# Kernel tuning notes

Hardware: AMD Instinct MI355X
Metric: run time of the kernel (lower is better)

The kernel has to match this reference:

```python
import jax, jax.numpy as jnp
import numpy as np

D_MODEL = 256
D_STATE = 64
HEADDIM = 64
EXPAND = 2
D_INNER = EXPAND * D_MODEL        # 512
D_SSM = D_INNER                   # 512
NGROUPS = 1
NHEADS = D_SSM // HEADDIM         # 8
CONV_DIM = D_SSM + 2 * NGROUPS * D_STATE   # 640
D_IN_PROJ = 2 * D_INNER + 2 * NGROUPS * D_STATE + NHEADS  # 1160
BATCH, Himg, Wimg = 8, 64, 64
EPS = 1e-5


def causal_dw_conv1d(x, w, b):
    """Depthwise causal conv1d + SiLU. x:(B,C,L), w:(C,K), b:(C,)"""
    K = w.shape[1]
    L = x.shape[-1]
    xp = jnp.pad(x, ((0, 0), (0, 0), (K - 1, 0)))
    y = b[None, :, None]
    for k in range(K):
        y = y + w[:, k][None, :, None] * xp[:, :, k:k + L]
    return jax.nn.silu(y)


def setup_inputs() -> dict:
    key = jax.random.key(0)
    ks = jax.random.split(key, 12)
    u = jax.random.normal(ks[0], (BATCH, D_MODEL, Himg, Wimg), jnp.float32)
    in_proj_w = jax.random.normal(ks[1], (D_IN_PROJ, D_MODEL), jnp.float32) * 0.02
    conv_dt_w = jax.random.normal(ks[2], (NHEADS, 4), jnp.float32) * 0.1
    # dt_bias via inverse-softplus of dt ~ logU(1e-3, 0.1) as in the module init
    dt0 = jnp.exp(jax.random.uniform(ks[3], (NHEADS,)) * (np.log(0.1) - np.log(0.001)) + np.log(0.001))
    dt_bias = dt0 + jnp.log(-jnp.expm1(-dt0))
    conv_xBC_w = jax.random.normal(ks[4], (CONV_DIM, 3), jnp.float32) * 0.1
    conv_xBC_b = jax.random.normal(ks[5], (CONV_DIM,), jnp.float32) * 0.02
    conv_z_w = jax.random.normal(ks[6], (D_SSM, 3), jnp.float32) * 0.1
    conv_z_b = jax.random.normal(ks[7], (D_SSM,), jnp.float32) * 0.02
    A_log = jnp.log(jax.random.uniform(ks[8], (NHEADS,), minval=1.0, maxval=16.0))
    D_param = jnp.ones((NHEADS,), jnp.float32)
    norm_w = jnp.ones((D_SSM,), jnp.float32)
    out_proj_w = jax.random.normal(ks[9], (D_MODEL, D_SSM, 3, 3), jnp.float32) * 0.02
    return {"u": u, "in_proj_w": in_proj_w, "conv_dt_w": conv_dt_w, "dt_bias": dt_bias,
            "conv_xBC_w": conv_xBC_w, "conv_xBC_b": conv_xBC_b,
            "conv_z_w": conv_z_w, "conv_z_b": conv_z_b,
            "A_log": A_log, "D_param": D_param, "norm_w": norm_w, "out_proj_w": out_proj_w}


def reference(u, in_proj_w, conv_dt_w, dt_bias, conv_xBC_w, conv_xBC_b,
              conv_z_w, conv_z_b, A_log, D_param, norm_w, out_proj_w):
    B, C, H, W = u.shape
    L = H * W
    # 1x1 conv in_proj -> (B, D_IN_PROJ, L)
    zxbcdt = jnp.einsum('oc,bchw->bohw', in_proj_w, u).reshape(B, D_IN_PROJ, L)
    z = zxbcdt[:, :D_SSM]                                  # (B, D_SSM, L)
    xBC = zxbcdt[:, D_SSM:D_SSM + CONV_DIM]                # (B, CONV_DIM, L)
    dt = zxbcdt[:, D_SSM + CONV_DIM:]                      # (B, NHEADS, L)

    A = -jnp.exp(A_log)                                    # (NHEADS,)
    dt = causal_dw_conv1d(dt, conv_dt_w, dt_bias)          # (B, H, L), silu'd
    xBC = causal_dw_conv1d(xBC, conv_xBC_w, conv_xBC_b)    # (B, CONV_DIM, L)

    x = xBC[:, :D_SSM]                                     # (B, D_SSM, L)
    Bm = jnp.transpose(xBC[:, D_SSM:D_SSM + D_STATE], (0, 2, 1))   # (B, L, N)
    Cm = jnp.transpose(xBC[:, D_SSM + D_STATE:], (0, 2, 1))        # (B, L, N)

    # x: (B, h*c, L) -> V: (B, h, L, c)
    V = jnp.transpose(x.reshape(B, NHEADS, HEADDIM, L), (0, 1, 3, 2))
    # dA = dt * A per head: (B, h, L, 1)
    dA = dt[:, :, :, None] * A[None, :, None, None]
    V_scaled = V * dA
    # non-causal linear attention duality (ngroups==1)
    KV = jnp.einsum('bln,bhld->bhnd', Bm, V_scaled)        # (B, h, N, d)
    y = jnp.einsum('bln,bhnd->bhld', Cm, KV) + V * D_param[None, :, None, None]
    y = jnp.transpose(y, (0, 2, 1, 3)).reshape(B, L, D_SSM)

    # gate branch
    zc = causal_dw_conv1d(z, conv_z_w, conv_z_b)           # (B, D_SSM, L)
    zc = jnp.transpose(zc, (0, 2, 1))                      # (B, L, D_SSM)
    # RMSNormGated, norm_before_gate=False: gate first then normalize
    yg = y * jax.nn.silu(zc)
    yn = yg * jax.lax.rsqrt(jnp.mean(yg * yg, axis=-1, keepdims=True) + EPS) * norm_w

    y_img = jnp.transpose(yn, (0, 2, 1)).reshape(B, D_SSM, H, W)
    out = jax.lax.conv_general_dilated(y_img, out_proj_w, (1, 1), 'SAME',
                                       dimension_numbers=('NCHW', 'OIHW', 'NCHW'))
    return out
```

## Files before the change

kernel.cpp:

```cpp
#include <hip/hip_runtime.h>
#include <math.h>


constexpr int BATCH  = 8;
constexpr int CIN    = 256;
constexpr int HH     = 64, WW = 64;
constexpr int L      = HH * WW;
constexpr int DPROJ  = 1160;
constexpr int DSSM   = 512;
constexpr int DSTATE = 64;
constexpr int NH     = 8;
constexpr int HD     = 64;
constexpr int CONVD  = 640;
constexpr int COUT   = 256;
constexpr float EPS  = 1e-5f;

typedef __attribute__((ext_vector_type(8))) short short8;
typedef __attribute__((ext_vector_type(4))) float f32x4;

static __device__ __forceinline__ float silu_f(float x) {
    return x / (1.f + __expf(-x));
}
static __device__ __forceinline__ float bf2f(unsigned short u) {
    return __uint_as_float(((unsigned)u) << 16);
}
static __device__ __forceinline__ unsigned short f2bf(float f) {
    unsigned x = __float_as_uint(f);
    unsigned r = (x + 0x7FFFu + ((x >> 16) & 1u)) >> 16;
    return (unsigned short)r;
}

static __device__ __forceinline__ void gl2lds16(const unsigned short* g, short* l) {
    __builtin_amdgcn_global_load_lds(
        (const __attribute__((address_space(1))) unsigned int*)g,
        (__attribute__((address_space(3))) unsigned int*)l, 16, 0, 0);
}

__global__ __launch_bounds__(256) void k_wb2(const float* __restrict__ W,
                                             unsigned short* __restrict__ Wt2) {
    int idx8 = blockIdx.x * 256 + threadIdx.x;
    int tile = idx8 >> 9;
    int within = (idx8 & 511) * 8;
    int row = within >> 5;
    int slp = (within >> 3) & 3;
    int oblk = tile >> 3, ks = tile & 7;
    int o = oblk * 128 + row;
    int c = ks * 32 + (slp ^ (row & 3)) * 8;
    unsigned short s[8] = {0, 0, 0, 0, 0, 0, 0, 0};
    if (o < DPROJ) {
        float4 v0 = *(const float4*)(W + (size_t)o * CIN + c);
        float4 v1 = *(const float4*)(W + (size_t)o * CIN + c + 4);
        s[0] = f2bf(v0.x); s[1] = f2bf(v0.y); s[2] = f2bf(v0.z); s[3] = f2bf(v0.w);
        s[4] = f2bf(v1.x); s[5] = f2bf(v1.y); s[6] = f2bf(v1.z); s[7] = f2bf(v1.w);
    }
    *(uint4*)(Wt2 + (size_t)tile * 4096 + within) = *(uint4*)s;
}

__global__ __launch_bounds__(256) void k_uT(const float* __restrict__ u,
                                            unsigned short* __restrict__ uTt) {
    __shared__ float Ts[32][33];
    int l0 = blockIdx.x * 32;
    int c0 = blockIdx.y * 32;
    int b  = blockIdx.z;
    int tid = threadIdx.x;
    {
        int r = tid >> 3, c4 = tid & 7;
        float4 v = *(const float4*)(u + ((size_t)b * CIN + c0 + r) * L + l0 + c4 * 4);
        Ts[r][c4 * 4 + 0] = v.x;
        Ts[r][c4 * 4 + 1] = v.y;
        Ts[r][c4 * 4 + 2] = v.z;
        Ts[r][c4 * 4 + 3] = v.w;
    }
    __syncthreads();
    {
        int lr = tid >> 3, cg = tid & 7;
        unsigned short s[4];
#pragma unroll
        for (int j = 0; j < 4; ++j) s[j] = f2bf(Ts[cg * 4 + j][lr]);
        int lg = l0 + lr;
        int tile = ((b * 32 + (lg >> 7)) << 3) + (c0 >> 5);
        int row = lg & 127;
        int slot = (cg >> 1) ^ (row & 3);
        size_t off = (size_t)tile * 4096 + row * 32 + slot * 8 + (cg & 1) * 4;
        *(uint2*)(uTt + off) = *(uint2*)s;
    }
}

__global__ __launch_bounds__(256) void k_wprep(const float* __restrict__ Wt,
                                               unsigned short* __restrict__ Wb2) {
    int i = blockIdx.x * 256 + threadIdx.x;
    int co = i >> 9, ci = i & 511;
    const float* src = Wt + (size_t)i * 9;
#pragma unroll
    for (int tap = 0; tap < 9; ++tap) {
        Wb2[(((size_t)tap * 64 + (ci >> 3)) * 256 + co) * 8 + (ci & 7)] = f2bf(src[tap]);
    }
}

__global__ __launch_bounds__(256) void k_inprojm(const unsigned short* __restrict__ Wt2,
                                                 const unsigned short* __restrict__ uTt,
                                                 unsigned short* __restrict__ zx) {
    __shared__ short Ab[2][4096];
    __shared__ short Bbuf[2][4096];
    int lblk = blockIdx.x, oblk = blockIdx.y, b = blockIdx.z;
    int tid = threadIdx.x, lane = tid & 63, w = tid >> 6;
    int laneN = lane & 15, laneK = lane >> 4;

    const unsigned short* At = uTt + (size_t)(b * 32 + lblk) * 8 * 4096;
    const unsigned short* Bt = Wt2 + (size_t)oblk * 8 * 4096;

    f32x4 acc[4][4];
#pragma unroll
    for (int mt = 0; mt < 4; ++mt)
#pragma unroll
        for (int nt = 0; nt < 4; ++nt) acc[mt][nt] = (f32x4){0.f, 0.f, 0.f, 0.f};

    gl2lds16(At + tid * 8,        &Ab[0][tid * 8]);
    gl2lds16(At + 2048 + tid * 8, &Ab[0][2048 + tid * 8]);
    gl2lds16(Bt + tid * 8,        &Bbuf[0][tid * 8]);
    gl2lds16(Bt + 2048 + tid * 8, &Bbuf[0][2048 + tid * 8]);
    __syncthreads();

    int arow = (w & 1) * 64;
    int brow = (w >> 1) * 64;
    int asl = (laneK ^ (laneN & 3)) * 8;

    int cur = 0;
    for (int ks = 0; ks < 8; ++ks) {
        if (ks < 7) {
            const unsigned short* an = At + (size_t)(ks + 1) * 4096;
            const unsigned short* bn = Bt + (size_t)(ks + 1) * 4096;
            int c2 = cur ^ 1;
            gl2lds16(an + tid * 8,        &Ab[c2][tid * 8]);
            gl2lds16(an + 2048 + tid * 8, &Ab[c2][2048 + tid * 8]);
            gl2lds16(bn + tid * 8,        &Bbuf[c2][tid * 8]);
            gl2lds16(bn + 2048 + tid * 8, &Bbuf[c2][2048 + tid * 8]);
        }
        short8 av[4], bv[4];
#pragma unroll
        for (int mt = 0; mt < 4; ++mt)
            av[mt] = *(const short8*)&Ab[cur][(arow + mt * 16 + laneN) * 32 + asl];
#pragma unroll
        for (int nt = 0; nt < 4; ++nt)
            bv[nt] = *(const short8*)&Bbuf[cur][(brow + nt * 16 + laneN) * 32 + asl];
#pragma unroll
        for (int mt = 0; mt < 4; ++mt)
#pragma unroll
            for (int nt = 0; nt < 4; ++nt)
                acc[mt][nt] = __builtin_amdgcn_mfma_f32_16x16x32_bf16(av[mt], bv[nt], acc[mt][nt], 0, 0, 0);
        __syncthreads();
        cur ^= 1;
    }

    unsigned short* zb = zx + (size_t)b * DPROJ * L;
    int lbase = lblk * 128 + arow;
#pragma unroll
    for (int nt = 0; nt < 4; ++nt) {
        int o = oblk * 128 + brow + nt * 16 + laneN;
        if (o < DPROJ) {
#pragma unroll
            for (int mt = 0; mt < 4; ++mt) {
                unsigned short s[4] = {f2bf(acc[mt][nt].x), f2bf(acc[mt][nt].y),
                                       f2bf(acc[mt][nt].z), f2bf(acc[mt][nt].w)};
                *(uint2*)(zb + (size_t)o * L + lbase + mt * 16 + laneK * 4) = *(uint2*)s;
            }
        }
    }
}

__global__ __launch_bounds__(256) void k_dtdA(const unsigned short* __restrict__ zx,
                                              const float* __restrict__ cw,
                                              const float* __restrict__ cb,
                                              const float* __restrict__ Alog,
                                              float* __restrict__ dA) {
    int idx = blockIdx.x * 256 + threadIdx.x;
    int l = idx & (L - 1);
    int h = (idx >> 12) & (NH - 1);
    int b = idx >> 15;
    const unsigned short* row = zx + ((size_t)b * DPROJ + DSSM + CONVD + h) * L;
    float y = cb[h];
#pragma unroll
    for (int k = 0; k < 4; ++k) {
        int ls = l + k - 3;
        if (ls >= 0) y += cw[h * 4 + k] * bf2f(row[ls]);
    }
    dA[idx] = silu_f(y) * (-__expf(Alog[h]));
}

__global__ __launch_bounds__(256) void k_xbc(const unsigned short* __restrict__ zx,
                                             const float* __restrict__ cw,
                                             const float* __restrict__ cb,
                                             unsigned short* __restrict__ xbc) {
    int idx = blockIdx.x * 256 + threadIdx.x;
    int lg = idx & (L / 8 - 1);
    int c  = (idx >> 9) % CONVD;
    int b  = idx / (CONVD * (L / 8));
    int l0 = lg * 8;
    const unsigned short* row = zx + ((size_t)b * DPROJ + DSSM + c) * L;
    float x[10];
    uint4 raw = *(const uint4*)(row + l0);
    const unsigned short* s = (const unsigned short*)&raw;
#pragma unroll
    for (int t = 0; t < 8; ++t) x[2 + t] = bf2f(s[t]);
    if (l0 > 0) { x[0] = bf2f(row[l0 - 2]); x[1] = bf2f(row[l0 - 1]); }
    else        { x[0] = 0.f; x[1] = 0.f; }
    float w0 = cw[c * 3 + 0], w1 = cw[c * 3 + 1], w2 = cw[c * 3 + 2], bb = cb[c];
    uint4 o;
    unsigned short* os = (unsigned short*)&o;
#pragma unroll
    for (int t = 0; t < 8; ++t) {
        float y = bb + w0 * x[t] + w1 * x[t + 1] + w2 * x[t + 2];
        os[t] = f2bf(silu_f(y));
    }
    *(uint4*)(xbc + ((size_t)b * CONVD + c) * L + l0) = o;
}

__global__ __launch_bounds__(256) void k_ct(const unsigned short* __restrict__ xbc,
                                            unsigned short* __restrict__ CT) {
    __shared__ short Ts[32][33];
    int l0 = blockIdx.x * 32;
    int n0 = blockIdx.y * 32;
    int b  = blockIdx.z;
    int tid = threadIdx.x;
    {
        int r = tid >> 3, q = tid & 7;
        uint2 v = *(const uint2*)(xbc + ((size_t)b * CONVD + DSSM + DSTATE + n0 + r) * L + l0 + q * 4);
        const unsigned short* s = (const unsigned short*)&v;
#pragma unroll
        for (int t = 0; t < 4; ++t) Ts[r][q * 4 + t] = (short)s[t];
    }
    __syncthreads();
    {
        int lr = tid >> 3, qn = tid & 7;
        unsigned short s[4];
#pragma unroll
        for (int t = 0; t < 4; ++t) s[t] = (unsigned short)Ts[qn * 4 + t][lr];
        *(uint2*)(CT + ((size_t)b * L + l0 + lr) * DSTATE + n0 + qn * 4) = *(uint2*)s;
    }
}

__global__ __launch_bounds__(256) void k_kvm(const unsigned short* __restrict__ xbc,
                                             const float* __restrict__ dA,
                                             float* __restrict__ pKV) {
    __shared__ float red[4][4096];
    int kc = blockIdx.x, h = blockIdx.y, b = blockIdx.z;
    int tid = threadIdx.x, lane = tid & 63, w = tid >> 6;
    int laneN = lane & 15, laneK = lane >> 4;

    const unsigned short* Bb = xbc + ((size_t)b * CONVD + DSSM) * L;
    const unsigned short* Vb = xbc + ((size_t)b * CONVD + h * HD) * L;
    const float* dAp = dA + ((size_t)b * NH + h) * L;

    f32x4 acc[4][4];
#pragma unroll
    for (int mt = 0; mt < 4; ++mt)
#pragma unroll
        for (int nt = 0; nt < 4; ++nt) acc[mt][nt] = (f32x4){0.f, 0.f, 0.f, 0.f};

    int kbase = kc * 512 + w * 128;
#pragma unroll
    for (int ks = 0; ks < 4; ++ks) {
        int kl = kbase + ks * 32 + laneK * 8;
        float4 da0 = *(const float4*)(dAp + kl);
        float4 da1 = *(const float4*)(dAp + kl + 4);
        float dav[8] = {da0.x, da0.y, da0.z, da0.w, da1.x, da1.y, da1.z, da1.w};
        short8 afr[4];
#pragma unroll
        for (int mt = 0; mt < 4; ++mt) {
            uint4 raw = *(const uint4*)(Bb + (size_t)(mt * 16 + laneN) * L + kl);
            const unsigned short* s = (const unsigned short*)&raw;
            short8 af;
#pragma unroll
            for (int j = 0; j < 8; ++j) af[j] = (short)f2bf(bf2f(s[j]) * dav[j]);
            afr[mt] = af;
        }
#pragma unroll
        for (int nt = 0; nt < 4; ++nt) {
            short8 bfr = *(const short8*)(Vb + (size_t)(nt * 16 + laneN) * L + kl);
#pragma unroll
            for (int mt = 0; mt < 4; ++mt)
                acc[mt][nt] = __builtin_amdgcn_mfma_f32_16x16x32_bf16(afr[mt], bfr, acc[mt][nt], 0, 0, 0);
        }
    }

#pragma unroll
    for (int mt = 0; mt < 4; ++mt)
#pragma unroll
        for (int nt = 0; nt < 4; ++nt)
#pragma unroll
            for (int j = 0; j < 4; ++j)
                red[w][(mt * 16 + laneK * 4 + j) * 64 + nt * 16 + laneN] = acc[mt][nt][j];
    __syncthreads();

    float* dst = pKV + (((size_t)(b * NH + h) * 8 + kc) * 4096);
#pragma unroll
    for (int q = 0; q < 4; ++q) {
        int off = q * 1024 + tid * 4;
        float4 s0 = *(const float4*)&red[0][off];
        float4 s1 = *(const float4*)&red[1][off];
        float4 s2 = *(const float4*)&red[2][off];
        float4 s3 = *(const float4*)&red[3][off];
        float4 r;
        r.x = s0.x + s1.x + s2.x + s3.x;
        r.y = s0.y + s1.y + s2.y + s3.y;
        r.z = s0.z + s1.z + s2.z + s3.z;
        r.w = s0.w + s1.w + s2.w + s3.w;
        *(float4*)(dst + off) = r;
    }
}

__global__ __launch_bounds__(256) void k_kvred(const float* __restrict__ pKV,
                                               float* __restrict__ KV) {
    int flat4 = blockIdx.x * 256 + threadIdx.x;
    int bh = flat4 >> 10;
    int nd = (flat4 & 1023) * 4;
    float4 r = make_float4(0.f, 0.f, 0.f, 0.f);
#pragma unroll
    for (int kc = 0; kc < 8; ++kc) {
        float4 v = *(const float4*)(pKV + ((size_t)bh * 8 + kc) * 4096 + nd);
        r.x += v.x; r.y += v.y; r.z += v.z; r.w += v.w;
    }
    *(float4*)(KV + (size_t)bh * 4096 + nd) = r;
}

__global__ __launch_bounds__(256) void k_kvT(const float* __restrict__ KV,
                                             unsigned short* __restrict__ KVt) {
    __shared__ float Ts[64][65];
    int bh = blockIdx.x;
    int tid = threadIdx.x;
    const float* src = KV + (size_t)bh * 4096;
#pragma unroll
    for (int j = 0; j < 16; ++j) {
        int idx = j * 256 + tid;
        Ts[idx >> 6][idx & 63] = src[idx];
    }
    __syncthreads();
    unsigned short* dst = KVt + (size_t)bh * 4096;
#pragma unroll
    for (int j = 0; j < 4; ++j) {
        int idx = j * 256 + tid;
        int d = idx >> 4, q = idx & 15;
        unsigned short s[4];
#pragma unroll
        for (int t = 0; t < 4; ++t) s[t] = f2bf(Ts[q * 4 + t][d]);
        *(uint2*)(dst + d * 64 + q * 4) = *(uint2*)s;
    }
}

__global__ __launch_bounds__(256) void k_y5am(const unsigned short* __restrict__ CT,
                                              const unsigned short* __restrict__ KVt,
                                              const unsigned short* __restrict__ xbc,
                                              const unsigned short* __restrict__ zx,
                                              const float* __restrict__ zw,
                                              const float* __restrict__ zb,
                                              const float* __restrict__ Dp,
                                              unsigned short* __restrict__ ygout) {
    int l0 = blockIdx.x * 128;
    int h  = blockIdx.y;
    int b  = blockIdx.z;
    int tid = threadIdx.x, lane = tid & 63, w = tid >> 6;
    int laneN = lane & 15, laneK = lane >> 4;
    int lw = l0 + w * 32;

    const unsigned short* ctb = CT + (size_t)b * L * DSTATE;
    const unsigned short* kvb = KVt + ((size_t)b * NH + h) * HD * DSTATE;

    f32x4 acc[2][4];
#pragma unroll
    for (int mt = 0; mt < 2; ++mt)
#pragma unroll
        for (int nt = 0; nt < 4; ++nt) acc[mt][nt] = (f32x4){0.f, 0.f, 0.f, 0.f};

#pragma unroll
    for (int ks = 0; ks < 2; ++ks) {
        int ko = ks * 32 + laneK * 8;
        short8 av[2], bv[4];
#pragma unroll
        for (int mt = 0; mt < 2; ++mt)
            av[mt] = *(const short8*)(ctb + (size_t)(lw + mt * 16 + laneN) * DSTATE + ko);
#pragma unroll
        for (int nt = 0; nt < 4; ++nt)
            bv[nt] = *(const short8*)(kvb + (size_t)(nt * 16 + laneN) * DSTATE + ko);
#pragma unroll
        for (int mt = 0; mt < 2; ++mt)
#pragma unroll
            for (int nt = 0; nt < 4; ++nt)
                acc[mt][nt] = __builtin_amdgcn_mfma_f32_16x16x32_bf16(av[mt], bv[nt], acc[mt][nt], 0, 0, 0);
    }

    const unsigned short* xb = xbc + (size_t)b * CONVD * L;
    float Dh = Dp[h];
#pragma unroll
    for (int nt = 0; nt < 4; ++nt) {
        int d = nt * 16 + laneN;
        int c = h * HD + d;
        float w0 = zw[c * 3 + 0], w1 = zw[c * 3 + 1], w2 = zw[c * 3 + 2];
        float bz = zb[c];
        const unsigned short* vrow = xb + (size_t)c * L;
        const unsigned short* zrow = zx + ((size_t)b * DPROJ + c) * L;
#pragma unroll
        for (int mt = 0; mt < 2; ++mt) {
            int lpos = lw + mt * 16 + laneK * 4;
            float v[4];
            {
                uint2 raw = *(const uint2*)(vrow + lpos);
                const unsigned short* s = (const unsigned short*)&raw;
#pragma unroll
                for (int t = 0; t < 4; ++t) v[t] = bf2f(s[t]);
            }
            float zv[8];
            if (lpos >= 4) {
                uint2 z0 = *(const uint2*)(zrow + lpos - 4);
                const unsigned short* s = (const unsigned short*)&z0;
#pragma unroll
                for (int t = 0; t < 4; ++t) zv[t] = bf2f(s[t]);
            } else {
                zv[0] = zv[1] = zv[2] = zv[3] = 0.f;
            }
            {
                uint2 z1 = *(const uint2*)(zrow + lpos);
                const unsigned short* s = (const unsigned short*)&z1;
#pragma unroll
                for (int t = 0; t < 4; ++t) zv[4 + t] = bf2f(s[t]);
            }
            unsigned short sp[4];
#pragma unroll
            for (int j = 0; j < 4; ++j) {
                float y = acc[mt][nt][j] + v[j] * Dh;
                float zy = bz + w0 * zv[j + 2] + w1 * zv[j + 3] + w2 * zv[j + 4];
                sp[j] = f2bf(y * silu_f(silu_f(zy)));
            }
            *(uint2*)(ygout + (size_t)b * DPROJ * L + (size_t)c * L + lpos) = *(uint2*)sp;
        }
    }
}

constexpr int R_LT = 32;

__global__ __launch_bounds__(256) void k_y5bT(const unsigned short* __restrict__ yg,
                                              const float* __restrict__ nw,
                                              unsigned short* __restrict__ ynT) {
    __shared__ float ygs[DSSM][R_LT + 1];
    __shared__ float red[8][R_LT];
    __shared__ float rs[R_LT];
    int l0 = blockIdx.x * R_LT;
    int b  = blockIdx.y;
    int tid = threadIdx.x;
    int ll = tid & 31, grp = tid >> 5;
    const unsigned short* ygb = yg + (size_t)b * DPROJ * L;
#pragma unroll
    for (int j = 0; j < 64; ++j) {
        int i = j * 256 + tid;
        int c = i >> 5, lc = i & 31;
        ygs[c][lc] = bf2f(ygb[(size_t)c * L + l0 + lc]);
    }
    __syncthreads();
    float ss = 0.f;
#pragma unroll
    for (int ci = 0; ci < 64; ++ci) {
        float t = ygs[grp * 64 + ci][ll];
        ss += t * t;
    }
    red[grp][ll] = ss;
    __syncthreads();
    if (tid < R_LT) {
        float s = 0.f;
#pragma unroll
        for (int g = 0; g < 8; ++g) s += red[g][tid];
        rs[tid] = rsqrtf(s * (1.f / DSSM) + EPS);
    }
    __syncthreads();
    int lc = tid & 31, cg = tid >> 5;
    float r = rs[lc];
    unsigned short* dst = ynT + ((size_t)b * L + l0 + lc) * DSSM + cg * 64;
#pragma unroll
    for (int j = 0; j < 8; ++j) {
        uint4 pk;
        unsigned short* sp = (unsigned short*)&pk;
#pragma unroll
        for (int t = 0; t < 8; ++t) {
            int c = cg * 64 + j * 8 + t;
            sp[t] = f2bf(ygs[c][lc] * r * nw[c]);
        }
        *(uint4*)(dst + j * 8) = pk;
    }
}

__global__ __launch_bounds__(256, 4) void k_conv3m(const unsigned short* __restrict__ ynT,
                                                   const unsigned short* __restrict__ Wb2,
                                                   float* __restrict__ out) {
    __shared__ short Alds[4 * 66 * 72];
    int h0  = blockIdx.x * 2;
    int co0 = blockIdx.y * 64;
    int b   = blockIdx.z;
    int tid  = threadIdx.x;
    int lane = tid & 63;
    int wid  = tid >> 6;
    int wm = wid >> 1, wn = wid & 1;
    int laneN = lane & 15, laneK = lane >> 4;

    f32x4 acc[4][2];
#pragma unroll
    for (int mt = 0; mt < 4; ++mt)
#pragma unroll
        for (int nt = 0; nt < 2; ++nt) acc[mt][nt] = (f32x4){0.f, 0.f, 0.f, 0.f};

    const unsigned short* ynb = ynT + (size_t)b * L * DSSM;

    const int a_wi1 = tid >> 2, a_sl = tid & 3;

    if (tid < 64) {
        int rw = tid >> 3, q = tid & 7;
        int r = rw >> 1, wi = (rw & 1) ? 65 : 0;
        *(uint4*)&Alds[(r * 66 + wi) * 72 + q * 8] = make_uint4(0u, 0u, 0u, 0u);
    }

    uint4 pA[8];
#pragma unroll
    for (int j = 0; j < 4; ++j) {
        int hrow = h0 - 1 + j;
        bool ok = (hrow >= 0 && hrow < HH);
        const unsigned short* src = ynb + (size_t)(hrow * WW + a_wi1) * DSSM;
#pragma unroll
        for (int s2 = 0; s2 < 2; ++s2) {
            pA[j * 2 + s2] = make_uint4(0u, 0u, 0u, 0u);
            if (ok) pA[j * 2 + s2] = *(const uint4*)(src + (a_sl + s2 * 4) * 8);
        }
    }

    const unsigned short* wbp =
        Wb2 + ((size_t)laneK * 256 + co0 + wn * 32 + laneN) * 8;

    for (int ci0 = 0; ci0 < DSSM; ci0 += 64) {
        __syncthreads();
#pragma unroll
        for (int j = 0; j < 4; ++j)
#pragma unroll
            for (int s2 = 0; s2 < 2; ++s2)
                *(uint4*)&Alds[(j * 66 + a_wi1 + 1) * 72 + (a_sl + s2 * 4) * 8] = pA[j * 2 + s2];
        __syncthreads();

        if (ci0 + 64 < DSSM) {
            int cin = ci0 + 64;
#pragma unroll
            for (int j = 0; j < 4; ++j) {
                int hrow = h0 - 1 + j;
                bool ok = (hrow >= 0 && hrow < HH);
                const unsigned short* src = ynb + (size_t)(hrow * WW + a_wi1) * DSSM + cin;
#pragma unroll
                for (int s2 = 0; s2 < 2; ++s2) {
                    pA[j * 2 + s2] = make_uint4(0u, 0u, 0u, 0u);
                    if (ok) pA[j * 2 + s2] = *(const uint4*)(src + (a_sl + s2 * 4) * 8);
                }
            }
        }

        const unsigned short* wbc = wbp + (size_t)(ci0 >> 3) * 2048;
        short8 bC[4];
#pragma unroll
        for (int ks = 0; ks < 2; ++ks)
#pragma unroll
            for (int nt = 0; nt < 2; ++nt)
                bC[ks * 2 + nt] = *(const short8*)(wbc + (size_t)ks * 8192 + nt * 128);
#pragma unroll
        for (int tap = 0; tap < 9; ++tap) {
            short8 bN[4];
#pragma unroll
            for (int q = 0; q < 4; ++q) bN[q] = bC[q];
            if (tap < 8) {
#pragma unroll
                for (int ks = 0; ks < 2; ++ks)
#pragma unroll
                    for (int nt = 0; nt < 2; ++nt)
                        bN[ks * 2 + nt] = *(const short8*)(wbc + (size_t)(tap + 1) * 131072 +
                                                          (size_t)ks * 8192 + nt * 128);
            }
            const int kh = tap / 3, kw = tap % 3;
#pragma unroll
            for (int ks = 0; ks < 2; ++ks) {
#pragma unroll
                for (int mt = 0; mt < 4; ++mt) {
                    short8 af = *(const short8*)&Alds[((wm + kh) * 66 + laneN + mt * 16 + kw) * 72 +
                                                      (laneK + ks * 4) * 8];
                    acc[mt][0] = __builtin_amdgcn_mfma_f32_16x16x32_bf16(af, bC[ks * 2 + 0], acc[mt][0], 0, 0, 0);
                    acc[mt][1] = __builtin_amdgcn_mfma_f32_16x16x32_bf16(af, bC[ks * 2 + 1], acc[mt][1], 0, 0, 0);
                }
            }
#pragma unroll
            for (int q = 0; q < 4; ++q) bC[q] = bN[q];
        }
    }

    float* ob = out + (size_t)b * COUT * L + (size_t)(h0 + wm) * WW;
#pragma unroll
    for (int mt = 0; mt < 4; ++mt) {
#pragma unroll
        for (int nt = 0; nt < 2; ++nt) {
            int co = co0 + wn * 32 + nt * 16 + laneN;
            float4 v = make_float4(acc[mt][nt].x, acc[mt][nt].y, acc[mt][nt].z, acc[mt][nt].w);
            *(float4*)(ob + (size_t)co * L + mt * 16 + laneK * 4) = v;
        }
    }
}

extern "C" void kernel_launch(void* const* d_in, const int* in_sizes, int n_in,
                              void* d_out, int out_size, void* d_ws, size_t ws_size,
                              hipStream_t stream) {
    const float* u          = (const float*)d_in[0];
    const float* in_proj_w  = (const float*)d_in[1];
    const float* conv_dt_w  = (const float*)d_in[2];
    const float* dt_bias    = (const float*)d_in[3];
    const float* conv_xBC_w = (const float*)d_in[4];
    const float* conv_xBC_b = (const float*)d_in[5];
    const float* conv_z_w   = (const float*)d_in[6];
    const float* conv_z_b   = (const float*)d_in[7];
    const float* A_log      = (const float*)d_in[8];
    const float* D_param    = (const float*)d_in[9];
    const float* norm_w     = (const float*)d_in[10];
    const float* out_w      = (const float*)d_in[11];
    float* out = (float*)d_out;

    const size_t n_zx  = (size_t)BATCH * DPROJ * L;
    const size_t n_xbc = (size_t)BATCH * CONVD * L;
    const size_t n_yn  = (size_t)BATCH * DSSM * L;
    const size_t n_dA  = (size_t)BATCH * NH * L;
    const size_t n_KV  = (size_t)BATCH * NH * DSTATE * HD;
    const size_t n_pKV = (size_t)BATCH * NH * 8 * DSTATE * HD;
    const size_t n_Wb2 = (size_t)9 * 64 * 256 * 8;
    const size_t n_ct  = (size_t)BATCH * L * DSTATE;
    const size_t n_kvt = (size_t)BATCH * NH * HD * DSTATE;
    const size_t need  = 2 * (n_zx + n_xbc + n_yn + n_Wb2 + n_ct + n_kvt)
                       + 4 * (n_dA + n_KV + n_pKV);
    if (ws_size < need) return;

    unsigned short* zx  = (unsigned short*)d_ws;
    unsigned short* xbc = zx + n_zx;
    unsigned short* ynT = xbc + n_xbc;
    float*          dAb = (float*)(ynT + n_yn);
    float*          KV  = dAb + n_dA;
    float*          pKV = KV + n_KV;
    unsigned short* Wb2 = (unsigned short*)(pKV + n_pKV);
    unsigned short* CT  = Wb2 + n_Wb2;
    unsigned short* KVt = CT + n_ct;
    unsigned short* uTt  = ynT;
    unsigned short* Wt2  = (unsigned short*)pKV;
    unsigned short* ygbuf = zx + (size_t)DSSM * L;

    k_wb2<<<160, 256, 0, stream>>>(in_proj_w, Wt2);

    dim3 gt(L / 32, CIN / 32, BATCH);
    k_uT<<<gt, 256, 0, stream>>>(u, uTt);

    k_wprep<<<(COUT * DSSM) / 256, 256, 0, stream>>>(out_w, Wb2);

    dim3 g1(L / 128, 10, BATCH);
    k_inprojm<<<g1, 256, 0, stream>>>(Wt2, uTt, zx);

    k_dtdA<<<BATCH * NH * L / 256, 256, 0, stream>>>(zx, conv_dt_w, dt_bias, A_log, dAb);

    k_xbc<<<BATCH * CONVD * (L / 8) / 256, 256, 0, stream>>>(zx, conv_xBC_w, conv_xBC_b, xbc);

    dim3 gct(L / 32, DSTATE / 32, BATCH);
    k_ct<<<gct, 256, 0, stream>>>(xbc, CT);

    dim3 g4(8, NH, BATCH);
    k_kvm<<<g4, 256, 0, stream>>>(xbc, dAb, pKV);
    k_kvred<<<256, 256, 0, stream>>>(pKV, KV);
    k_kvT<<<BATCH * NH, 256, 0, stream>>>(KV, KVt);

    dim3 g5(L / 128, NH, BATCH);
    k_y5am<<<g5, 256, 0, stream>>>(CT, KVt, xbc, zx, conv_z_w, conv_z_b, D_param, ygbuf);

    dim3 g5b(L / R_LT, BATCH);
    k_y5bT<<<g5b, 256, 0, stream>>>(ygbuf, norm_w, ynT);

    dim3 g6(HH / 2, COUT / 64, BATCH);
    k_conv3m<<<g6, 256, 0, stream>>>(ynT, Wb2, out);
}
```

Before: 248.0 us.

## Fuse KV reduction with transpose, and fuse y-gating with RMSNorm into one kernel

The partial-KV reduction is merged into the transpose/bf16 conversion kernel, and the y computation (C·KV plus D skip and z gate) is fused with the RMSNorm into a single kernel. Each block now covers all 8 heads for 32 positions, so the row sum of squares is reduced in registers, by shuffles and through a small shared array, instead of passing through an intermediate yg buffer. This removes two launches and the round trip of the gated activations through global memory. The cost is that ynT is written with scattered 2-byte stores strided by DSSM, and the KV reduction now runs on only 64 blocks.

```diff
diff --git a/kernel.cpp b/kernel.cpp
--- a/kernel.cpp
+++ b/kernel.cpp
@@ -309,30 +309,19 @@
     }
 }
 
-__global__ __launch_bounds__(256) void k_kvred(const float* __restrict__ pKV,
-                                               float* __restrict__ KV) {
-    int flat4 = blockIdx.x * 256 + threadIdx.x;
-    int bh = flat4 >> 10;
-    int nd = (flat4 & 1023) * 4;
-    float4 r = make_float4(0.f, 0.f, 0.f, 0.f);
-#pragma unroll
-    for (int kc = 0; kc < 8; ++kc) {
-        float4 v = *(const float4*)(pKV + ((size_t)bh * 8 + kc) * 4096 + nd);
-        r.x += v.x; r.y += v.y; r.z += v.z; r.w += v.w;
-    }
-    *(float4*)(KV + (size_t)bh * 4096 + nd) = r;
-}
-
-__global__ __launch_bounds__(256) void k_kvT(const float* __restrict__ KV,
-                                             unsigned short* __restrict__ KVt) {
+__global__ __launch_bounds__(256) void k_kvrt(const float* __restrict__ pKV,
+                                              unsigned short* __restrict__ KVt) {
     __shared__ float Ts[64][65];
     int bh = blockIdx.x;
     int tid = threadIdx.x;
-    const float* src = KV + (size_t)bh * 4096;
+    const float* src = pKV + (size_t)bh * 8 * 4096;
 #pragma unroll
     for (int j = 0; j < 16; ++j) {
         int idx = j * 256 + tid;
-        Ts[idx >> 6][idx & 63] = src[idx];
+        float s = 0.f;
+#pragma unroll
+        for (int kc = 0; kc < 8; ++kc) s += src[(size_t)kc * 4096 + idx];
+        Ts[idx >> 6][idx & 63] = s;
     }
     __syncthreads();
     unsigned short* dst = KVt + (size_t)bh * 4096;
@@ -347,60 +336,65 @@
     }
 }
 
-__global__ __launch_bounds__(256) void k_y5am(const unsigned short* __restrict__ CT,
-                                              const unsigned short* __restrict__ KVt,
-                                              const unsigned short* __restrict__ xbc,
-                                              const unsigned short* __restrict__ zx,
-                                              const float* __restrict__ zw,
-                                              const float* __restrict__ zb,
-                                              const float* __restrict__ Dp,
-                                              unsigned short* __restrict__ ygout) {
-    int l0 = blockIdx.x * 128;
-    int h  = blockIdx.y;
-    int b  = blockIdx.z;
+__global__ __launch_bounds__(256) void k_y5n(const unsigned short* __restrict__ CT,
+                                             const unsigned short* __restrict__ KVt,
+                                             const unsigned short* __restrict__ xbc,
+                                             const unsigned short* __restrict__ zx,
+                                             const float* __restrict__ zw,
+                                             const float* __restrict__ zb,
+                                             const float* __restrict__ Dp,
+                                             const float* __restrict__ nw,
+                                             unsigned short* __restrict__ ynT) {
+    __shared__ float red[32][4];
+    int l0 = blockIdx.x * 32;
+    int b  = blockIdx.y;
     int tid = threadIdx.x, lane = tid & 63, w = tid >> 6;
     int laneN = lane & 15, laneK = lane >> 4;
-    int lw = l0 + w * 32;
 
     const unsigned short* ctb = CT + (size_t)b * L * DSTATE;
-    const unsigned short* kvb = KVt + ((size_t)b * NH + h) * HD * DSTATE;
-
-    f32x4 acc[2][4];
+    const unsigned short* xb  = xbc + (size_t)b * CONVD * L;
+
+    f32x4 acc[2][8];
 #pragma unroll
     for (int mt = 0; mt < 2; ++mt)
 #pragma unroll
-        for (int nt = 0; nt < 4; ++nt) acc[mt][nt] = (f32x4){0.f, 0.f, 0.f, 0.f};
+        for (int nt = 0; nt < 8; ++nt) acc[mt][nt] = (f32x4){0.f, 0.f, 0.f, 0.f};
 
 #pragma unroll
     for (int ks = 0; ks < 2; ++ks) {
         int ko = ks * 32 + laneK * 8;
-        short8 av[2], bv[4];
+        short8 av[2];
 #pragma unroll
         for (int mt = 0; mt < 2; ++mt)
-            av[mt] = *(const short8*)(ctb + (size_t)(lw + mt * 16 + laneN) * DSTATE + ko);
-#pragma unroll
-        for (int nt = 0; nt < 4; ++nt)
-            bv[nt] = *(const short8*)(kvb + (size_t)(nt * 16 + laneN) * DSTATE + ko);
-#pragma unroll
-        for (int mt = 0; mt < 2; ++mt)
-#pragma unroll
-            for (int nt = 0; nt < 4; ++nt)
-                acc[mt][nt] = __builtin_amdgcn_mfma_f32_16x16x32_bf16(av[mt], bv[nt], acc[mt][nt], 0, 0, 0);
-    }
-
-    const unsigned short* xb = xbc + (size_t)b * CONVD * L;
-    float Dh = Dp[h];
-#pragma unroll
-    for (int nt = 0; nt < 4; ++nt) {
-        int d = nt * 16 + laneN;
-        int c = h * HD + d;
+            av[mt] = *(const short8*)(ctb + (size_t)(l0 + mt * 16 + laneN) * DSTATE + ko);
+#pragma unroll
+        for (int nt = 0; nt < 8; ++nt) {
+            int head = w * 2 + (nt >> 2);
+            const unsigned short* kvb = KVt + (size_t)(b * NH + head) * (HD * DSTATE);
+            short8 bv = *(const short8*)(kvb + (size_t)((nt & 3) * 16 + laneN) * DSTATE + ko);
+            acc[0][nt] = __builtin_amdgcn_mfma_f32_16x16x32_bf16(av[0], bv, acc[0][nt], 0, 0, 0);
+            acc[1][nt] = __builtin_amdgcn_mfma_f32_16x16x32_bf16(av[1], bv, acc[1][nt], 0, 0, 0);
+        }
+    }
+
+    float ps[2][4];
+#pragma unroll
+    for (int mt = 0; mt < 2; ++mt)
+#pragma unroll
+        for (int j = 0; j < 4; ++j) ps[mt][j] = 0.f;
+
+#pragma unroll
+    for (int nt = 0; nt < 8; ++nt) {
+        int head = w * 2 + (nt >> 2);
+        int c = head * 64 + (nt & 3) * 16 + laneN;
+        float Dh = Dp[head];
         float w0 = zw[c * 3 + 0], w1 = zw[c * 3 + 1], w2 = zw[c * 3 + 2];
         float bz = zb[c];
         const unsigned short* vrow = xb + (size_t)c * L;
         const unsigned short* zrow = zx + ((size_t)b * DPROJ + c) * L;
 #pragma unroll
         for (int mt = 0; mt < 2; ++mt) {
-            int lpos = lw + mt * 16 + laneK * 4;
+            int lpos = l0 + mt * 16 + laneK * 4;
             float v[4];
             {
                 uint2 raw = *(const uint2*)(vrow + lpos);
@@ -423,66 +417,56 @@
 #pragma unroll
                 for (int t = 0; t < 4; ++t) zv[4 + t] = bf2f(s[t]);
             }
-            unsigned short sp[4];
 #pragma unroll
             for (int j = 0; j < 4; ++j) {
                 float y = acc[mt][nt][j] + v[j] * Dh;
                 float zy = bz + w0 * zv[j + 2] + w1 * zv[j + 3] + w2 * zv[j + 4];
-                sp[j] = f2bf(y * silu_f(silu_f(zy)));
-            }
-            *(uint2*)(ygout + (size_t)b * DPROJ * L + (size_t)c * L + lpos) = *(uint2*)sp;
-        }
-    }
-}
-
-constexpr int R_LT = 32;
-
-__global__ __launch_bounds__(256) void k_y5bT(const unsigned short* __restrict__ yg,
-                                              const float* __restrict__ nw,
-                                              unsigned short* __restrict__ ynT) {
-    __shared__ float ygs[DSSM][R_LT + 1];
-    __shared__ float red[8][R_LT];
-    __shared__ float rs[R_LT];
-    int l0 = blockIdx.x * R_LT;
-    int b  = blockIdx.y;
-    int tid = threadIdx.x;
-    int ll = tid & 31, grp = tid >> 5;
-    const unsigned short* ygb = yg + (size_t)b * DPROJ * L;
-#pragma unroll
-    for (int j = 0; j < 64; ++j) {
-        int i = j * 256 + tid;
-        int c = i >> 5, lc = i & 31;
-        ygs[c][lc] = bf2f(ygb[(size_t)c * L + l0 + lc]);
+                float yg = y * silu_f(silu_f(zy));
+                ps[mt][j] += yg * yg;
+                acc[mt][nt][j] = yg;
+            }
+        }
+    }
+
+#pragma unroll
+    for (int m = 1; m <= 8; m <<= 1) {
+#pragma unroll
+        for (int mt = 0; mt < 2; ++mt)
+#pragma unroll
+            for (int j = 0; j < 4; ++j)
+                ps[mt][j] += __shfl_xor(ps[mt][j], m, 64);
+    }
+    if (laneN == 0) {
+#pragma unroll
+        for (int mt = 0; mt < 2; ++mt)
+#pragma unroll
+            for (int j = 0; j < 4; ++j)
+                red[mt * 16 + laneK * 4 + j][w] = ps[mt][j];
     }
     __syncthreads();
-    float ss = 0.f;
-#pragma unroll
-    for (int ci = 0; ci < 64; ++ci) {
-        float t = ygs[grp * 64 + ci][ll];
-        ss += t * t;
-    }
-    red[grp][ll] = ss;
-    __syncthreads();
-    if (tid < R_LT) {
-        float s = 0.f;
-#pragma unroll
-        for (int g = 0; g < 8; ++g) s += red[g][tid];
-        rs[tid] = rsqrtf(s * (1.f / DSSM) + EPS);
-    }
-    __syncthreads();
-    int lc = tid & 31, cg = tid >> 5;
-    float r = rs[lc];
-    unsigned short* dst = ynT + ((size_t)b * L + l0 + lc) * DSSM + cg * 64;
-#pragma unroll
-    for (int j = 0; j < 8; ++j) {
-        uint4 pk;
-        unsigned short* sp = (unsigned short*)&pk;
-#pragma unroll
-        for (int t = 0; t < 8; ++t) {
-            int c = cg * 64 + j * 8 + t;
-            sp[t] = f2bf(ygs[c][lc] * r * nw[c]);
-        }
-        *(uint4*)(dst + j * 8) = pk;
+
+    float rr[2][4];
+#pragma unroll
+    for (int mt = 0; mt < 2; ++mt)
+#pragma unroll
+        for (int j = 0; j < 4; ++j) {
+            int ll = mt * 16 + laneK * 4 + j;
+            float s = red[ll][0] + red[ll][1] + red[ll][2] + red[ll][3];
+            rr[mt][j] = rsqrtf(s * (1.f / DSSM) + EPS);
+        }
+
+#pragma unroll
+    for (int nt = 0; nt < 8; ++nt) {
+        int c = (w * 2 + (nt >> 2)) * 64 + (nt & 3) * 16 + laneN;
+        float nwc = nw[c];
+#pragma unroll
+        for (int mt = 0; mt < 2; ++mt) {
+            int lpos = l0 + mt * 16 + laneK * 4;
+            unsigned short* dst = ynT + ((size_t)b * L + lpos) * DSSM + c;
+#pragma unroll
+            for (int j = 0; j < 4; ++j)
+                dst[(size_t)j * DSSM] = f2bf(acc[mt][nt][j] * rr[mt][j] * nwc);
+        }
     }
 }
 
@@ -624,27 +608,24 @@
     const size_t n_xbc = (size_t)BATCH * CONVD * L;
     const size_t n_yn  = (size_t)BATCH * DSSM * L;
     const size_t n_dA  = (size_t)BATCH * NH * L;
-    const size_t n_KV  = (size_t)BATCH * NH * DSTATE * HD;
     const size_t n_pKV = (size_t)BATCH * NH * 8 * DSTATE * HD;
     const size_t n_Wb2 = (size_t)9 * 64 * 256 * 8;
     const size_t n_ct  = (size_t)BATCH * L * DSTATE;
     const size_t n_kvt = (size_t)BATCH * NH * HD * DSTATE;
     const size_t need  = 2 * (n_zx + n_xbc + n_yn + n_Wb2 + n_ct + n_kvt)
-                       + 4 * (n_dA + n_KV + n_pKV);
+                       + 4 * (n_dA + n_pKV);
     if (ws_size < need) return;
 
     unsigned short* zx  = (unsigned short*)d_ws;
     unsigned short* xbc = zx + n_zx;
     unsigned short* ynT = xbc + n_xbc;
     float*          dAb = (float*)(ynT + n_yn);
-    float*          KV  = dAb + n_dA;
-    float*          pKV = KV + n_KV;
+    float*          pKV = dAb + n_dA;
     unsigned short* Wb2 = (unsigned short*)(pKV + n_pKV);
     unsigned short* CT  = Wb2 + n_Wb2;
     unsigned short* KVt = CT + n_ct;
-    unsigned short* uTt  = ynT;
-    unsigned short* Wt2  = (unsigned short*)pKV;
-    unsigned short* ygbuf = zx + (size_t)DSSM * L;
+    unsigned short* uTt = ynT;
+    unsigned short* Wt2 = (unsigned short*)pKV;
 
     k_wb2<<<160, 256, 0, stream>>>(in_proj_w, Wt2);
 
@@ -665,14 +646,10 @@
 
     dim3 g4(8, NH, BATCH);
     k_kvm<<<g4, 256, 0, stream>>>(xbc, dAb, pKV);
-    k_kvred<<<256, 256, 0, stream>>>(pKV, KV);
-    k_kvT<<<BATCH * NH, 256, 0, stream>>>(KV, KVt);
-
-    dim3 g5(L / 128, NH, BATCH);
-    k_y5am<<<g5, 256, 0, stream>>>(CT, KVt, xbc, zx, conv_z_w, conv_z_b, D_param, ygbuf);
-
-    dim3 g5b(L / R_LT, BATCH);
-    k_y5bT<<<g5b, 256, 0, stream>>>(ygbuf, norm_w, ynT);
+    k_kvrt<<<BATCH * NH, 256, 0, stream>>>(pKV, KVt);
+
+    dim3 g5(L / 32, BATCH);
+    k_y5n<<<g5, 256, 0, stream>>>(CT, KVt, xbc, zx, conv_z_w, conv_z_b, D_param, norm_w, ynT);
 
     dim3 g6(HH / 2, COUT / 64, BATCH);
     k_conv3m<<<g6, 256, 0, stream>>>(ynT, Wb2, out);
```

Result: slower. 257.9 us (+4.0%).
